# Performance work log

Measured on AMD Instinct MI355X. Metric: run time of the kernel, lower is better.

The kernel has to match this reference:

```python
import jax, jax.numpy as jnp
import numpy as np
import math

EMBED_DIM = 1024
NUM_HEADS = 16
HEAD_DIM = EMBED_DIM // NUM_HEADS
BATCH = 2
SEQ = 2048


def setup_inputs() -> dict:
    key = jax.random.key(0)
    ks = jax.random.split(key, 9)
    s = 1.0 / math.sqrt(EMBED_DIM)
    return {
        "x": jax.random.normal(ks[0], (BATCH, SEQ, EMBED_DIM), jnp.float32),
        "Wq": jax.random.normal(ks[1], (EMBED_DIM, EMBED_DIM), jnp.float32) * s,
        "bq": jnp.zeros((EMBED_DIM,), jnp.float32),
        "Wk": jax.random.normal(ks[2], (EMBED_DIM, EMBED_DIM), jnp.float32) * s,
        "bk": jnp.zeros((EMBED_DIM,), jnp.float32),
        "Wv": jax.random.normal(ks[3], (EMBED_DIM, EMBED_DIM), jnp.float32) * s,
        "bv": jnp.zeros((EMBED_DIM,), jnp.float32),
        "Wo": jax.random.normal(ks[4], (EMBED_DIM, EMBED_DIM), jnp.float32) * s,
        "bo": jnp.zeros((EMBED_DIM,), jnp.float32),
    }


def _rope_tables(seq_len, dim, dtype):
    inv_freq = 1.0 / (10000.0 ** (jnp.arange(0, dim, 2, dtype=jnp.float32) / dim))
    t = jnp.arange(seq_len, dtype=jnp.float32)
    freqs = jnp.einsum("i,j->ij", t, inv_freq)          # [S, D/2]
    emb = jnp.concatenate([freqs, freqs], axis=-1)       # [S, D]
    return jnp.cos(emb).astype(dtype), jnp.sin(emb).astype(dtype)


def _rotate_half(x):
    x1, x2 = jnp.split(x, 2, axis=-1)
    return jnp.concatenate([-x2, x1], axis=-1)


def _apply_rope(x, cos, sin):
    # x: [B, S, H, D]; cos/sin: [S, D] -> broadcast over batch & heads
    cos = cos[None, :, None, :]
    sin = sin[None, :, None, :]
    return x * cos + _rotate_half(x) * sin


def reference(x, Wq, bq, Wk, bk, Wv, bv, Wo, bo):
    B, S, E = x.shape
    H, D = NUM_HEADS, HEAD_DIM
    q = (x @ Wq + bq).reshape(B, S, H, D)
    k = (x @ Wk + bk).reshape(B, S, H, D)
    v = (x @ Wv + bv).reshape(B, S, H, D)
    cos, sin = _rope_tables(S, D, x.dtype)
    q = _apply_rope(q, cos, sin)
    k = _apply_rope(k, cos, sin)
    scale = 1.0 / math.sqrt(D)
    # scores: [B, H, S, S]
    scores = jnp.einsum("bqhd,bkhd->bhqk", q, k) * scale
    attn = jax.nn.softmax(scores, axis=-1)
    ctx = jnp.einsum("bhqk,bkhd->bqhd", attn, v).reshape(B, S, E)
    return ctx @ Wo + bo
```

## Files before the change

kernel.cpp:

```cpp
#include <hip/hip_runtime.h>
#include <math.h>

#define B_ 2
#define S_ 2048
#define E_ 1024
#define H_ 16
#define D_ 64
#define M_ (B_*S_)

typedef _Float16 f16x8  __attribute__((ext_vector_type(8)));
typedef _Float16 f16x4v __attribute__((ext_vector_type(4)));
typedef __fp16   h16x2  __attribute__((ext_vector_type(2)));
typedef float    f32x4  __attribute__((ext_vector_type(4)));

__device__ __forceinline__ ushort f2h(float f) {
    _Float16 h = (_Float16)f;
    return __builtin_bit_cast(ushort, h);
}

__device__ __forceinline__ void gload_lds16(const ushort* g, ushort* l) {
    __builtin_amdgcn_global_load_lds(
        (const __attribute__((address_space(1))) unsigned int*)g,
        (__attribute__((address_space(3))) unsigned int*)l, 16, 0, 0);
}

__device__ __forceinline__ float exp2_fast(float x) {
    return __builtin_amdgcn_exp2f(x);
}

__global__ void prep_kernel(const float* __restrict__ x,
                            const float* __restrict__ W0, const float* __restrict__ W1,
                            const float* __restrict__ W2, const float* __restrict__ W3,
                            ushort* __restrict__ xf, ushort* __restrict__ WT,
                            float* __restrict__ ct, float* __restrict__ st)
{
    const int bid = blockIdx.x;
    const int tid = threadIdx.x;
    __shared__ float tile[32][33];

    if (bid < 4096) {
        const int z = bid >> 10, rem = bid & 1023;
        const int k0 = (rem >> 5) * 32, nb = (rem & 31) * 32;
        const float* W = (z == 0) ? W0 : (z == 1) ? W1 : (z == 2) ? W2 : W3;
        const size_t zoff = (size_t)z * E_ * E_;
        const int tx = tid & 31, ty = tid >> 5;
        #pragma unroll
        for (int i = 0; i < 4; i++) {
            int r = i * 8 + ty;
            tile[r][tx] = W[(size_t)(k0 + r) * E_ + nb + tx];
        }
        __syncthreads();
        #pragma unroll
        for (int i = 0; i < 4; i++) {
            int r = i * 8 + ty;
            WT[zoff + (size_t)(nb + r) * E_ + k0 + tx] = f2h(tile[tx][r]);
        }
    } else if (bid < 8192) {
        const int i = (bid - 4096) * 1024 + tid * 4;
        float4 v = *(const float4*)&x[i];
        *(ushort4*)&xf[i] = make_ushort4(f2h(v.x), f2h(v.y), f2h(v.z), f2h(v.w));
    } else {
        const int i = (bid - 8192) * 256 + tid;
        const int j = i & 31, pos = i >> 5;
        float invf = (float)pow(10000.0, -(double)j / 32.0);
        float ang  = (float)pos * invf;
        ct[i] = (float)cos((double)ang);
        st[i] = (float)sin((double)ang);
    }
}

#define GBM 128
#define GBN 128
#define GBK 32
#define LOG2E 1.44269504088896340736f

__global__ __launch_bounds__(256, 3)
void gemm_f16(const ushort* __restrict__ A, const ushort* __restrict__ WTp,
              const float* __restrict__ b0, const float* __restrict__ b1,
              const float* __restrict__ b2,
              const float* __restrict__ ct, const float* __restrict__ st,
              ushort* __restrict__ outQ, ushort* __restrict__ outK,
              ushort* __restrict__ outV, float* __restrict__ outF,
              int force_mode)
{
    __shared__ __align__(16) ushort lA[3][GBM * GBK];
    __shared__ __align__(16) ushort lB[3][GBN * GBK];

    const int tid  = threadIdx.x;
    const int wv   = tid >> 6, lane = tid & 63;
    const int c    = lane & 15, qd = lane >> 4;
    const int rh   = wv >> 1, chn = wv & 1;

    const int mode = (force_mode >= 0) ? force_mode : (int)blockIdx.z;
    const size_t zoff = (force_mode >= 0) ? 0 : (size_t)blockIdx.z * (E_ * E_);
    const ushort* Bt = WTp + zoff;

    const int m0 = (blockIdx.x & 31) * GBM;
    const int n0 = (blockIdx.x >> 5) * GBN;

    const ushort* gsrc = (wv < 2) ? A : Bt;
    const int rowbase = ((wv < 2) ? m0 : n0) + (wv & 1) * 64;
    const int lofs = (wv & 1) * 64 * GBK;
    const int srow = lane >> 2;
    const int soct = (lane & 3) * 8;

    f32x4 acc[4][4] = {};

    #pragma unroll
    for (int pt = 0; pt < 2; pt++) {
        ushort* dst = ((wv < 2) ? &lA[pt][0] : &lB[pt][0]) + lofs;
        const int k0i = pt * GBK;
        #pragma unroll
        for (int cc = 0; cc < 4; cc++) {
            const ushort* g = gsrc + (size_t)(rowbase + cc * 16 + srow) * E_ + k0i + soct;
            gload_lds16(g, dst + cc * 512);
        }
    }
    __builtin_amdgcn_s_waitcnt(0x0F74);
    __builtin_amdgcn_s_barrier();

    for (int t = 0; t < E_ / GBK; t++) {
        if (t + 2 < E_ / GBK) {
            const int bi = (t + 2) % 3;
            const int k0i = (t + 2) * GBK;
            ushort* dst = ((wv < 2) ? &lA[bi][0] : &lB[bi][0]) + lofs;
            #pragma unroll
            for (int cc = 0; cc < 4; cc++) {
                const ushort* g = gsrc + (size_t)(rowbase + cc * 16 + srow) * E_ + k0i + soct;
                gload_lds16(g, dst + cc * 512);
            }
        }

        const ushort* Ab = lA[t % 3];
        const ushort* Bb = lB[t % 3];

        f16x8 af[4], bf[4];
        #pragma unroll
        for (int mt = 0; mt < 4; mt++)
            af[mt] = *(const f16x8*)&Ab[(rh * 64 + mt * 16 + c) * GBK + qd * 8];
        #pragma unroll
        for (int nt = 0; nt < 4; nt++)
            bf[nt] = *(const f16x8*)&Bb[(chn * 64 + nt * 16 + c) * GBK + qd * 8];
        #pragma unroll
        for (int mt = 0; mt < 4; mt++)
            #pragma unroll
            for (int nt = 0; nt < 4; nt++)
                acc[mt][nt] = __builtin_amdgcn_mfma_f32_16x16x32_f16(af[mt], bf[nt], acc[mt][nt], 0, 0, 0);

        if (t < E_ / GBK - 2) {
            __builtin_amdgcn_s_waitcnt(0x0F74);
            __builtin_amdgcn_s_barrier();
        } else if (t == E_ / GBK - 2) {
            __builtin_amdgcn_s_waitcnt(0x0F70);
            __builtin_amdgcn_s_barrier();
        }
    }

    const float* bias = (mode == 0) ? b0 : (mode == 1) ? b1 : (mode == 2) ? b2 : b0;
    const int colbase = n0 + chn * 64;

    if (mode == 3) {
        #pragma unroll
        for (int mt = 0; mt < 4; mt++)
            #pragma unroll
            for (int r = 0; r < 4; r++) {
                const int row = m0 + rh * 64 + mt * 16 + qd * 4 + r;
                #pragma unroll
                for (int nt = 0; nt < 4; nt++) {
                    const int col = colbase + nt * 16 + c;
                    outF[(size_t)row * E_ + col] = acc[mt][nt][r] + bias[col];
                }
            }
    } else if (mode == 2) {
        const int hd = colbase >> 6;
        #pragma unroll
        for (int mt = 0; mt < 4; mt++)
            #pragma unroll
            for (int r = 0; r < 4; r++) {
                const int row = m0 + rh * 64 + mt * 16 + qd * 4 + r;
                const int bb = row >> 11, sl = row & (S_ - 1);
                const size_t base = (size_t)(bb * H_ + hd) * (S_ * D_)
                                  + (sl >> 6) * 4096 + ((sl >> 4) & 3) * 1024 + (sl & 15);
                #pragma unroll
                for (int nt = 0; nt < 4; nt++) {
                    const int d = nt * 16 + c;
                    outV[base + d * 16] = f2h(acc[mt][nt][r] + bias[colbase + d]);
                }
            }
    } else {
        ushort* O = (mode == 0) ? outQ : outK;
        const float sc = (mode == 0) ? 0.125f * LOG2E : 1.0f;
        #pragma unroll
        for (int mt = 0; mt < 4; mt++)
            #pragma unroll
            for (int r = 0; r < 4; r++) {
                const int row = m0 + rh * 64 + mt * 16 + qd * 4 + r;
                const int pos = row & (S_ - 1);
                const int sw = row & 7;
                #pragma unroll
                for (int p = 0; p < 2; p++) {
                    const int j32 = p * 16 + c;
                    const float cth = ct[pos * 32 + j32], sth = st[pos * 32 + j32];
                    const float v1 = acc[mt][p][r]     + bias[colbase + p * 16 + c];
                    const float v2 = acc[mt][p + 2][r] + bias[colbase + (p + 2) * 16 + c];
                    const float o1 = (v1 * cth - v2 * sth) * sc;
                    const float o2 = (v2 * cth + v1 * sth) * sc;
                    const int cd1 = p * 16 + c, cd2 = cd1 + 32;
                    O[(size_t)row * E_ + colbase + (((cd1 >> 3) ^ sw) * 8) + (cd1 & 7)] = f2h(o1);
                    O[(size_t)row * E_ + colbase + (((cd2 >> 3) ^ sw) * 8) + (cd2 & 7)] = f2h(o2);
                }
            }
    }
}

__global__ __launch_bounds__(256, 3)
void attn_mfma(const ushort* __restrict__ Qf, const ushort* __restrict__ Kf,
               const ushort* __restrict__ Vfg, ushort* __restrict__ ctxf)
{
    __shared__ __align__(16) ushort L[16384];

    const int tid = threadIdx.x;
    const int wv = tid >> 6, lane = tid & 63;
    const int c = lane & 15, qd = lane >> 4;
    const int cs = c & 7;

    const int xcd = blockIdx.x & 7, ii = blockIdx.x >> 3;
    const int bh = xcd * 4 + (ii & 3);
    const int qtb = ii >> 2;
    const int b = bh >> 4, h = bh & 15;
    const int q0 = qtb * 64;

    const size_t qrow0 = (size_t)b * S_ + q0;
    const size_t krow0 = (size_t)b * S_;
    const size_t vbase = (size_t)bh * (S_ * D_);

    const int l8 = lane >> 3, l7 = lane & 7;

    #pragma unroll
    for (int j = 0; j < 2; j++) {
        const int row = wv * 16 + j * 8 + l8;
        gload_lds16(Qf + (qrow0 + row) * E_ + h * 64 + l7 * 8, &L[wv * 1024 + j * 512]);
    }
    __syncthreads();
    f16x8 qfrag[4][2];
    #pragma unroll
    for (int qt = 0; qt < 4; qt++)
        #pragma unroll
        for (int kc = 0; kc < 2; kc++)
            qfrag[qt][kc] = *(const f16x8*)&L[(qt * 16 + c) * 64 + (((kc * 4 + qd) ^ cs) * 8)];
    __syncthreads();

    f32x4 acc[4][4] = {};
    float lsum[4] = {0.f, 0.f, 0.f, 0.f};

    ushort* const myL = &L[wv * 4096];

    #pragma unroll
    for (int j = 0; j < 2; j++)
        gload_lds16(Kf + (krow0 + wv * 16 + j * 8 + l8) * E_ + h * 64 + l7 * 8,
                    myL + j * 512);
    #pragma unroll
    for (int j = 0; j < 2; j++)
        gload_lds16(Vfg + vbase + wv * 1024 + j * 512 + lane * 8,
                    myL + 1024 + j * 512);

    #pragma unroll 1
    for (int t = 0; t < 32; t++) {
        if (t < 31) {
            ushort* nb = myL + ((t + 1) & 1) * 2048;
            const int k0n = (t + 1) * 64;
            #pragma unroll
            for (int j = 0; j < 2; j++)
                gload_lds16(Kf + (krow0 + k0n + wv * 16 + j * 8 + l8) * E_ + h * 64 + l7 * 8,
                            nb + j * 512);
            #pragma unroll
            for (int j = 0; j < 2; j++)
                gload_lds16(Vfg + vbase + (t + 1) * 4096 + wv * 1024 + j * 512 + lane * 8,
                            nb + 1024 + j * 512);
            __builtin_amdgcn_s_waitcnt(0x0F74);
        } else {
            __builtin_amdgcn_s_waitcnt(0x0F70);
        }

        const ushort* kb = myL + (t & 1) * 2048;
        const ushort* vb = kb + 1024;

        f16x8 kfr[2];
        #pragma unroll
        for (int kc = 0; kc < 2; kc++)
            kfr[kc] = *(const f16x8*)&kb[c * 64 + (((kc * 4 + qd) ^ cs) * 8)];

        f16x4v bfrag[4];
        #pragma unroll
        for (int qt = 0; qt < 4; qt++) {
            f32x4 s = {};
            s = __builtin_amdgcn_mfma_f32_16x16x32_f16(kfr[0], qfrag[qt][0], s, 0, 0, 0);
            s = __builtin_amdgcn_mfma_f32_16x16x32_f16(kfr[1], qfrag[qt][1], s, 0, 0, 0);
            const float p0 = exp2_fast(s[0]), p1 = exp2_fast(s[1]);
            const float p2 = exp2_fast(s[2]), p3 = exp2_fast(s[3]);
            lsum[qt] += (p0 + p1) + (p2 + p3);
            h16x2 lo = __builtin_amdgcn_cvt_pkrtz(p0, p1);
            h16x2 hi = __builtin_amdgcn_cvt_pkrtz(p2, p3);
            uint2 u;
            u.x = __builtin_bit_cast(unsigned int, lo);
            u.y = __builtin_bit_cast(unsigned int, hi);
            bfrag[qt] = __builtin_bit_cast(f16x4v, u);
        }

        #pragma unroll
        for (int dt = 0; dt < 4; dt++) {
            f16x4v vfr = *(const f16x4v*)&vb[(dt * 16 + c) * 16 + qd * 4];
            #pragma unroll
            for (int qt = 0; qt < 4; qt++)
                acc[dt][qt] = __builtin_amdgcn_mfma_f32_16x16x16f16(vfr, bfrag[qt], acc[dt][qt], 0, 0, 0);
        }
    }

    __syncthreads();

    float* red = (float*)&L[0];
    float* lsr = (float*)&L[8192];

    #pragma unroll
    for (int qt = 0; qt < 4; qt++) {
        float v = lsum[qt];
        v += __shfl_xor(v, 16);
        v += __shfl_xor(v, 32);
        lsum[qt] = v;
    }
    if (lane < 16) {
        #pragma unroll
        for (int qt = 0; qt < 4; qt++) lsr[wv * 64 + qt * 16 + lane] = lsum[qt];
    }

    f32x4 own[4];
    #pragma unroll
    for (int qt = 0; qt < 4; qt++)
        own[qt] = (wv == 0) ? acc[0][qt] : (wv == 1) ? acc[1][qt]
                : (wv == 2) ? acc[2][qt] : acc[3][qt];

    #pragma unroll
    for (int r = 1; r < 4; r++) {
        const int ds = (wv + r) & 3;
        #pragma unroll
        for (int qt = 0; qt < 4; qt++) {
            f32x4 sv = (ds == 0) ? acc[0][qt] : (ds == 1) ? acc[1][qt]
                     : (ds == 2) ? acc[2][qt] : acc[3][qt];
            *(f32x4*)&red[ds * 1024 + qt * 256 + lane * 4] = sv;
        }
        __syncthreads();
        #pragma unroll
        for (int qt = 0; qt < 4; qt++)
            own[qt] += *(const f32x4*)&red[wv * 1024 + qt * 256 + lane * 4];
        if (r < 3) __syncthreads();
    }

    float inv[4];
    #pragma unroll
    for (int qt = 0; qt < 4; qt++) {
        const int q = qt * 16 + c;
        inv[qt] = 1.0f / (lsr[q] + lsr[64 + q] + lsr[128 + q] + lsr[192 + q]);
    }

    const size_t obase = qrow0 * E_ + h * 64 + wv * 16 + qd * 4;
    #pragma unroll
    for (int qt = 0; qt < 4; qt++) {
        f32x4 v = own[qt];
        const float iq = inv[qt];
        ushort4 o = make_ushort4(f2h(v[0] * iq), f2h(v[1] * iq),
                                 f2h(v[2] * iq), f2h(v[3] * iq));
        *(ushort4*)&ctxf[obase + (size_t)(qt * 16 + c) * E_] = o;
    }
}

extern "C" void kernel_launch(void* const* d_in, const int* in_sizes, int n_in,
                              void* d_out, int out_size, void* d_ws, size_t ws_size,
                              hipStream_t stream)
{
    const float* x  = (const float*)d_in[0];
    const float* Wq = (const float*)d_in[1];
    const float* bq = (const float*)d_in[2];
    const float* Wk = (const float*)d_in[3];
    const float* bk = (const float*)d_in[4];
    const float* Wv = (const float*)d_in[5];
    const float* bv = (const float*)d_in[6];
    const float* Wo = (const float*)d_in[7];
    const float* bo = (const float*)d_in[8];
    float* out = (float*)d_out;

    ushort* Qb = (ushort*)d_ws;
    ushort* Kb = Qb + (size_t)M_ * E_;
    ushort* Vf = Kb + (size_t)M_ * E_;
    ushort* xf = Vf + (size_t)M_ * E_;
    ushort* WT = xf + (size_t)M_ * E_;
    float*  ct = (float*)(WT + (size_t)4 * E_ * E_);
    float*  st = ct + S_ * 32;
    ushort* ctxf = Qb;

    hipLaunchKernelGGL(prep_kernel, dim3(8448), dim3(256), 0, stream,
                       x, Wq, Wk, Wv, Wo, xf, WT, ct, st);

    hipLaunchKernelGGL(gemm_f16, dim3(256, 1, 3), dim3(256), 0, stream,
                       xf, WT, bq, bk, bv, ct, st,
                       Qb, Kb, Vf, (float*)nullptr, -1);

    hipLaunchKernelGGL(attn_mfma, dim3(B_ * H_ * (S_ / 64)), dim3(256), 0, stream,
                       Qb, Kb, Vf, ctxf);

    hipLaunchKernelGGL(gemm_f16, dim3(256), dim3(256), 0, stream,
                       ctxf, WT + (size_t)3 * E_ * E_, bo, bo, bo, ct, st,
                       (ushort*)nullptr, (ushort*)nullptr, (ushort*)nullptr, out, 3);
}
```

Baseline: 187.6 us.

## Load K/V fragments directly from global into registers, drop LDS staging

The attention kernel no longer stages Q, K and V tiles through LDS with global_load_lds double buffering. Each lane now reads its MFMA fragments straight from global memory, with one-step register prefetch for K. The XOR swizzle on the Q/K projection store is removed to match the new linear reads, and occupancy is raised to 4 blocks per CU now that LDS use is smaller. The aim is to cut LDS traffic and block-level synchronisation, but it relies on cache hits for the strided, less coalesced global loads, and V has no prefetch to hide its latency.

```diff
diff --git a/kernel.cpp b/kernel.cpp
--- a/kernel.cpp
+++ b/kernel.cpp
@@ -196,7 +196,6 @@
             for (int r = 0; r < 4; r++) {
                 const int row = m0 + rh * 64 + mt * 16 + qd * 4 + r;
                 const int pos = row & (S_ - 1);
-                const int sw = row & 7;
                 #pragma unroll
                 for (int p = 0; p < 2; p++) {
                     const int j32 = p * 16 + c;
@@ -205,24 +204,23 @@
                     const float v2 = acc[mt][p + 2][r] + bias[colbase + (p + 2) * 16 + c];
                     const float o1 = (v1 * cth - v2 * sth) * sc;
                     const float o2 = (v2 * cth + v1 * sth) * sc;
-                    const int cd1 = p * 16 + c, cd2 = cd1 + 32;
-                    O[(size_t)row * E_ + colbase + (((cd1 >> 3) ^ sw) * 8) + (cd1 & 7)] = f2h(o1);
-                    O[(size_t)row * E_ + colbase + (((cd2 >> 3) ^ sw) * 8) + (cd2 & 7)] = f2h(o2);
+                    O[(size_t)row * E_ + colbase + j32]      = f2h(o1);
+                    O[(size_t)row * E_ + colbase + j32 + 32] = f2h(o2);
                 }
             }
     }
 }
 
-__global__ __launch_bounds__(256, 3)
+__global__ __launch_bounds__(256, 4)
 void attn_mfma(const ushort* __restrict__ Qf, const ushort* __restrict__ Kf,
                const ushort* __restrict__ Vfg, ushort* __restrict__ ctxf)
 {
-    __shared__ __align__(16) ushort L[16384];
+    __shared__ __align__(16) float red[4 * 1024];
+    __shared__ float lsr[256];
 
     const int tid = threadIdx.x;
     const int wv = tid >> 6, lane = tid & 63;
     const int c = lane & 15, qd = lane >> 4;
-    const int cs = c & 7;
 
     const int xcd = blockIdx.x & 7, ii = blockIdx.x >> 3;
     const int bh = xcd * 4 + (ii & 3);
@@ -234,68 +232,42 @@
     const size_t krow0 = (size_t)b * S_;
     const size_t vbase = (size_t)bh * (S_ * D_);
 
-    const int l8 = lane >> 3, l7 = lane & 7;
-
-    #pragma unroll
-    for (int j = 0; j < 2; j++) {
-        const int row = wv * 16 + j * 8 + l8;
-        gload_lds16(Qf + (qrow0 + row) * E_ + h * 64 + l7 * 8, &L[wv * 1024 + j * 512]);
-    }
-    __syncthreads();
     f16x8 qfrag[4][2];
     #pragma unroll
     for (int qt = 0; qt < 4; qt++)
         #pragma unroll
         for (int kc = 0; kc < 2; kc++)
-            qfrag[qt][kc] = *(const f16x8*)&L[(qt * 16 + c) * 64 + (((kc * 4 + qd) ^ cs) * 8)];
-    __syncthreads();
+            qfrag[qt][kc] = *(const f16x8*)&Qf[(qrow0 + qt * 16 + c) * E_
+                                               + h * 64 + (kc * 4 + qd) * 8];
 
     f32x4 acc[4][4] = {};
     float lsum[4] = {0.f, 0.f, 0.f, 0.f};
 
-    ushort* const myL = &L[wv * 4096];
-
-    #pragma unroll
-    for (int j = 0; j < 2; j++)
-        gload_lds16(Kf + (krow0 + wv * 16 + j * 8 + l8) * E_ + h * 64 + l7 * 8,
-                    myL + j * 512);
-    #pragma unroll
-    for (int j = 0; j < 2; j++)
-        gload_lds16(Vfg + vbase + wv * 1024 + j * 512 + lane * 8,
-                    myL + 1024 + j * 512);
+    const ushort* kp = Kf + (krow0 + wv * 16 + c) * E_ + h * 64 + qd * 8;
+    const ushort* vp = Vfg + vbase + wv * 1024 + c * 16 + qd * 4;
+
+    f16x8 kcur0 = *(const f16x8*)(kp);
+    f16x8 kcur1 = *(const f16x8*)(kp + 32);
 
     #pragma unroll 1
     for (int t = 0; t < 32; t++) {
-        if (t < 31) {
-            ushort* nb = myL + ((t + 1) & 1) * 2048;
-            const int k0n = (t + 1) * 64;
-            #pragma unroll
-            for (int j = 0; j < 2; j++)
-                gload_lds16(Kf + (krow0 + k0n + wv * 16 + j * 8 + l8) * E_ + h * 64 + l7 * 8,
-                            nb + j * 512);
-            #pragma unroll
-            for (int j = 0; j < 2; j++)
-                gload_lds16(Vfg + vbase + (t + 1) * 4096 + wv * 1024 + j * 512 + lane * 8,
-                            nb + 1024 + j * 512);
-            __builtin_amdgcn_s_waitcnt(0x0F74);
-        } else {
-            __builtin_amdgcn_s_waitcnt(0x0F70);
-        }
-
-        const ushort* kb = myL + (t & 1) * 2048;
-        const ushort* vb = kb + 1024;
-
-        f16x8 kfr[2];
-        #pragma unroll
-        for (int kc = 0; kc < 2; kc++)
-            kfr[kc] = *(const f16x8*)&kb[c * 64 + (((kc * 4 + qd) ^ cs) * 8)];
+        const int tn = (t < 31) ? t + 1 : t;
+        const ushort* kn = kp + (size_t)tn * (64 * E_);
+        f16x8 knxt0 = *(const f16x8*)(kn);
+        f16x8 knxt1 = *(const f16x8*)(kn + 32);
+
+        const ushort* vt = vp + (size_t)t * 4096;
+        f16x4v vfr0 = *(const f16x4v*)(vt);
+        f16x4v vfr1 = *(const f16x4v*)(vt + 256);
+        f16x4v vfr2 = *(const f16x4v*)(vt + 512);
+        f16x4v vfr3 = *(const f16x4v*)(vt + 768);
 
         f16x4v bfrag[4];
         #pragma unroll
         for (int qt = 0; qt < 4; qt++) {
             f32x4 s = {};
-            s = __builtin_amdgcn_mfma_f32_16x16x32_f16(kfr[0], qfrag[qt][0], s, 0, 0, 0);
-            s = __builtin_amdgcn_mfma_f32_16x16x32_f16(kfr[1], qfrag[qt][1], s, 0, 0, 0);
+            s = __builtin_amdgcn_mfma_f32_16x16x32_f16(kcur0, qfrag[qt][0], s, 0, 0, 0);
+            s = __builtin_amdgcn_mfma_f32_16x16x32_f16(kcur1, qfrag[qt][1], s, 0, 0, 0);
             const float p0 = exp2_fast(s[0]), p1 = exp2_fast(s[1]);
             const float p2 = exp2_fast(s[2]), p3 = exp2_fast(s[3]);
             lsum[qt] += (p0 + p1) + (p2 + p3);
@@ -308,18 +280,15 @@
         }
 
         #pragma unroll
-        for (int dt = 0; dt < 4; dt++) {
-            f16x4v vfr = *(const f16x4v*)&vb[(dt * 16 + c) * 16 + qd * 4];
-            #pragma unroll
-            for (int qt = 0; qt < 4; qt++)
-                acc[dt][qt] = __builtin_amdgcn_mfma_f32_16x16x16f16(vfr, bfrag[qt], acc[dt][qt], 0, 0, 0);
-        }
-    }
-
-    __syncthreads();
-
-    float* red = (float*)&L[0];
-    float* lsr = (float*)&L[8192];
+        for (int qt = 0; qt < 4; qt++) {
+            acc[0][qt] = __builtin_amdgcn_mfma_f32_16x16x16f16(vfr0, bfrag[qt], acc[0][qt], 0, 0, 0);
+            acc[1][qt] = __builtin_amdgcn_mfma_f32_16x16x16f16(vfr1, bfrag[qt], acc[1][qt], 0, 0, 0);
+            acc[2][qt] = __builtin_amdgcn_mfma_f32_16x16x16f16(vfr2, bfrag[qt], acc[2][qt], 0, 0, 0);
+            acc[3][qt] = __builtin_amdgcn_mfma_f32_16x16x16f16(vfr3, bfrag[qt], acc[3][qt], 0, 0, 0);
+        }
+
+        kcur0 = knxt0; kcur1 = knxt1;
+    }
 
     #pragma unroll
     for (int qt = 0; qt < 4; qt++) {
```

Measured after the change: 224.4 us. 19.6% more time.

## Switch PV product to 16x16x32 MFMA with 32-key V tiles and swizzled layout

Applied to the files above, without the earlier changes.

The V tensor is re-laid out in the projection epilogue into 32-key groups with an XOR swizzle, so the attention kernel can feed the P·V product through the 16x16x32 f16 MFMA instead of 16x16x16. Each loop iteration now handles two 16-key score halves whose probabilities are packed into one 8-wide fragment, and loads of K and V are staggered between the halves. The PV section is also wrapped in s_setprio. LDS use per block rises from 32 KB to 48 KB, which may reduce occupancy against the launch bound of 3 blocks per CU.

```diff
diff --git a/kernel.cpp b/kernel.cpp
--- a/kernel.cpp
+++ b/kernel.cpp
@@ -173,18 +173,21 @@
             }
     } else if (mode == 2) {
         const int hd = colbase >> 6;
+        const int xr = c & 3;
         #pragma unroll
         for (int mt = 0; mt < 4; mt++)
             #pragma unroll
             for (int r = 0; r < 4; r++) {
                 const int row = m0 + rh * 64 + mt * 16 + qd * 4 + r;
                 const int bb = row >> 11, sl = row & (S_ - 1);
+                const int g  = sl >> 5, k32 = sl & 31;
+                const int q2 = (k32 >> 2) & 3, kh = k32 >> 4, kj = k32 & 3;
                 const size_t base = (size_t)(bb * H_ + hd) * (S_ * D_)
-                                  + (sl >> 6) * 4096 + ((sl >> 4) & 3) * 1024 + (sl & 15);
+                                  + g * 2048 + ((q2 ^ xr) << 3) + kh * 4 + kj;
                 #pragma unroll
                 for (int nt = 0; nt < 4; nt++) {
                     const int d = nt * 16 + c;
-                    outV[base + d * 16] = f2h(acc[mt][nt][r] + bias[colbase + d]);
+                    outV[base + (size_t)d * 32] = f2h(acc[mt][nt][r] + bias[colbase + d]);
                 }
             }
     } else {
@@ -217,7 +220,7 @@
 void attn_mfma(const ushort* __restrict__ Qf, const ushort* __restrict__ Kf,
                const ushort* __restrict__ Vfg, ushort* __restrict__ ctxf)
 {
-    __shared__ __align__(16) ushort L[16384];
+    __shared__ __align__(16) ushort L[24576];
 
     const int tid = threadIdx.x;
     const int wv = tid >> 6, lane = tid & 63;
@@ -253,67 +256,95 @@
     f32x4 acc[4][4] = {};
     float lsum[4] = {0.f, 0.f, 0.f, 0.f};
 
-    ushort* const myL = &L[wv * 4096];
+    ushort* const myL = &L[wv * 6144];
+    const int vxo = (qd ^ (c & 3)) << 3;
 
     #pragma unroll
     for (int j = 0; j < 2; j++)
-        gload_lds16(Kf + (krow0 + wv * 16 + j * 8 + l8) * E_ + h * 64 + l7 * 8,
+        gload_lds16(Kf + (krow0 + wv * 32 + j * 8 + l8) * E_ + h * 64 + l7 * 8,
                     myL + j * 512);
     #pragma unroll
     for (int j = 0; j < 2; j++)
-        gload_lds16(Vfg + vbase + wv * 1024 + j * 512 + lane * 8,
-                    myL + 1024 + j * 512);
+        gload_lds16(Vfg + vbase + (size_t)wv * 2048 + j * 512 + lane * 8,
+                    myL + 2048 + j * 512);
 
     #pragma unroll 1
-    for (int t = 0; t < 32; t++) {
-        if (t < 31) {
-            ushort* nb = myL + ((t + 1) & 1) * 2048;
-            const int k0n = (t + 1) * 64;
+    for (int T = 0; T < 16; T++) {
+        uint4 bfu[4];
+
+        {
+            const int g1 = T * 4 + wv;
+            ushort* vdst = myL + 2048 + (T & 1) * 2048 + 1024;
             #pragma unroll
             for (int j = 0; j < 2; j++)
-                gload_lds16(Kf + (krow0 + k0n + wv * 16 + j * 8 + l8) * E_ + h * 64 + l7 * 8,
-                            nb + j * 512);
+                gload_lds16(Kf + (krow0 + g1 * 32 + 16 + j * 8 + l8) * E_ + h * 64 + l7 * 8,
+                            myL + 1024 + j * 512);
             #pragma unroll
             for (int j = 0; j < 2; j++)
-                gload_lds16(Vfg + vbase + (t + 1) * 4096 + wv * 1024 + j * 512 + lane * 8,
-                            nb + 1024 + j * 512);
+                gload_lds16(Vfg + vbase + (size_t)g1 * 2048 + 1024 + j * 512 + lane * 8,
+                            vdst + j * 512);
             __builtin_amdgcn_s_waitcnt(0x0F74);
-        } else {
-            __builtin_amdgcn_s_waitcnt(0x0F70);
-        }
-
-        const ushort* kb = myL + (t & 1) * 2048;
-        const ushort* vb = kb + 1024;
-
-        f16x8 kfr[2];
-        #pragma unroll
-        for (int kc = 0; kc < 2; kc++)
-            kfr[kc] = *(const f16x8*)&kb[c * 64 + (((kc * 4 + qd) ^ cs) * 8)];
-
-        f16x4v bfrag[4];
-        #pragma unroll
-        for (int qt = 0; qt < 4; qt++) {
-            f32x4 s = {};
-            s = __builtin_amdgcn_mfma_f32_16x16x32_f16(kfr[0], qfrag[qt][0], s, 0, 0, 0);
-            s = __builtin_amdgcn_mfma_f32_16x16x32_f16(kfr[1], qfrag[qt][1], s, 0, 0, 0);
-            const float p0 = exp2_fast(s[0]), p1 = exp2_fast(s[1]);
-            const float p2 = exp2_fast(s[2]), p3 = exp2_fast(s[3]);
-            lsum[qt] += (p0 + p1) + (p2 + p3);
-            h16x2 lo = __builtin_amdgcn_cvt_pkrtz(p0, p1);
-            h16x2 hi = __builtin_amdgcn_cvt_pkrtz(p2, p3);
-            uint2 u;
-            u.x = __builtin_bit_cast(unsigned int, lo);
-            u.y = __builtin_bit_cast(unsigned int, hi);
-            bfrag[qt] = __builtin_bit_cast(f16x4v, u);
-        }
-
+
+            const ushort* kb = myL;
+            f16x8 kf0 = *(const f16x8*)&kb[c * 64 + ((qd ^ cs) * 8)];
+            f16x8 kf1 = *(const f16x8*)&kb[c * 64 + (((4 + qd) ^ cs) * 8)];
+            #pragma unroll
+            for (int qt = 0; qt < 4; qt++) {
+                f32x4 s = {};
+                s = __builtin_amdgcn_mfma_f32_16x16x32_f16(kf0, qfrag[qt][0], s, 0, 0, 0);
+                s = __builtin_amdgcn_mfma_f32_16x16x32_f16(kf1, qfrag[qt][1], s, 0, 0, 0);
+                const float p0 = exp2_fast(s[0]), p1 = exp2_fast(s[1]);
+                const float p2 = exp2_fast(s[2]), p3 = exp2_fast(s[3]);
+                lsum[qt] += (p0 + p1) + (p2 + p3);
+                bfu[qt].x = __builtin_bit_cast(unsigned int, __builtin_amdgcn_cvt_pkrtz(p0, p1));
+                bfu[qt].y = __builtin_bit_cast(unsigned int, __builtin_amdgcn_cvt_pkrtz(p2, p3));
+            }
+        }
+
+        {
+            if (T < 15) {
+                const int g2 = (T + 1) * 4 + wv;
+                ushort* vdst = myL + 2048 + ((T + 1) & 1) * 2048;
+                #pragma unroll
+                for (int j = 0; j < 2; j++)
+                    gload_lds16(Kf + (krow0 + g2 * 32 + j * 8 + l8) * E_ + h * 64 + l7 * 8,
+                                myL + j * 512);
+                #pragma unroll
+                for (int j = 0; j < 2; j++)
+                    gload_lds16(Vfg + vbase + (size_t)g2 * 2048 + j * 512 + lane * 8,
+                                vdst + j * 512);
+                __builtin_amdgcn_s_waitcnt(0x0F74);
+            } else {
+                __builtin_amdgcn_s_waitcnt(0x0F70);
+            }
+
+            const ushort* kb = myL + 1024;
+            f16x8 kf0 = *(const f16x8*)&kb[c * 64 + ((qd ^ cs) * 8)];
+            f16x8 kf1 = *(const f16x8*)&kb[c * 64 + (((4 + qd) ^ cs) * 8)];
+            #pragma unroll
+            for (int qt = 0; qt < 4; qt++) {
+                f32x4 s = {};
+                s = __builtin_amdgcn_mfma_f32_16x16x32_f16(kf0, qfrag[qt][0], s, 0, 0, 0);
+                s = __builtin_amdgcn_mfma_f32_16x16x32_f16(kf1, qfrag[qt][1], s, 0, 0, 0);
+                const float p0 = exp2_fast(s[0]), p1 = exp2_fast(s[1]);
+                const float p2 = exp2_fast(s[2]), p3 = exp2_fast(s[3]);
+                lsum[qt] += (p0 + p1) + (p2 + p3);
+                bfu[qt].z = __builtin_bit_cast(unsigned int, __builtin_amdgcn_cvt_pkrtz(p0, p1));
+                bfu[qt].w = __builtin_bit_cast(unsigned int, __builtin_amdgcn_cvt_pkrtz(p2, p3));
+            }
+        }
+
+        const ushort* vb = myL + 2048 + (T & 1) * 2048;
+        __builtin_amdgcn_s_setprio(1);
         #pragma unroll
         for (int dt = 0; dt < 4; dt++) {
-            f16x4v vfr = *(const f16x4v*)&vb[(dt * 16 + c) * 16 + qd * 4];
+            f16x8 vfr = *(const f16x8*)&vb[(dt * 16 + c) * 32 + vxo];
             #pragma unroll
             for (int qt = 0; qt < 4; qt++)
-                acc[dt][qt] = __builtin_amdgcn_mfma_f32_16x16x16f16(vfr, bfrag[qt], acc[dt][qt], 0, 0, 0);
-        }
+                acc[dt][qt] = __builtin_amdgcn_mfma_f32_16x16x32_f16(
+                    vfr, __builtin_bit_cast(f16x8, bfu[qt]), acc[dt][qt], 0, 0, 0);
+        }
+        __builtin_amdgcn_s_setprio(0);
     }
 
     __syncthreads();
```

After: 179.4 us. 4.3% less time.
